# Optimization experiments

Measured on AMD Instinct MI355X. Metric: run time of the kernel, lower is better.

Reference implementation:

```python
import jax, jax.numpy as jnp
import numpy as np

DIM = 512
HEADS = 8
DIM_HEAD = 64
HIDDEN = HEADS * DIM_HEAD
SCALE = DIM_HEAD ** -0.5


def rmsnorm_ch(x, g):
    # F.normalize over channel dim (axis=1), then * g * sqrt(C)
    # x: [b, c, l], g: [c]
    n = jnp.maximum(jnp.linalg.norm(x, axis=1, keepdims=True), 1e-12)
    c = x.shape[1]
    return (x / n) * g[None, :, None] * (c ** 0.5)


def setup_inputs() -> dict:
    key = jax.random.key(0)
    ks = jax.random.split(key, 6)
    b, l = 8, 4096
    x = jax.random.normal(ks[0], (b, DIM, l), dtype=jnp.float32)
    g_in = jnp.ones((DIM,), dtype=jnp.float32)
    # conv1d kernel_size=1 == matmul; kaiming-ish init scale
    w_qkv = jax.random.normal(ks[1], (3 * HIDDEN, DIM), dtype=jnp.float32) * (1.0 / np.sqrt(DIM))
    w_out = jax.random.normal(ks[2], (DIM, HIDDEN), dtype=jnp.float32) * (1.0 / np.sqrt(HIDDEN))
    b_out = jax.random.normal(ks[3], (DIM,), dtype=jnp.float32) * 0.01
    g_out = jnp.ones((DIM,), dtype=jnp.float32)
    return {"x": x, "g_in": g_in, "w_qkv": w_qkv, "w_out": w_out, "b_out": b_out, "g_out": g_out}


def reference(x, g_in, w_qkv, w_out, b_out, g_out):
    b, c, l = x.shape
    residual = x
    xn = rmsnorm_ch(x, g_in)                       # [b, c, l]
    qkv = jnp.einsum('oc,bcl->bol', w_qkv, xn)     # [b, 3*hidden, l]
    q, k, v = jnp.split(qkv, 3, axis=1)            # each [b, hidden, l]
    def to_heads(t):
        return t.reshape(b, HEADS, DIM_HEAD, l)    # [b, h, d, l]
    q, k, v = to_heads(q), to_heads(k), to_heads(v)
    q = jax.nn.softmax(q, axis=2) * SCALE          # softmax over head-dim d
    k = jax.nn.softmax(k, axis=3)                  # softmax over sequence l
    context = jnp.einsum('bhdn,bhen->bhde', k, v)  # [b, h, d, e]
    out = jnp.einsum('bhde,bhdn->bhen', context, q)  # [b, h, e, l]
    out = out.reshape(b, HIDDEN, l)
    o = jnp.einsum('ch,bhl->bcl', w_out, out) + b_out[None, :, None]
    o = rmsnorm_ch(o, g_out)
    return o + residual
```

## Files before the change

### kernel.cpp

```cpp
#include <hip/hip_runtime.h>


#define BB 8
#define CC 512
#define LL 4096
#define HH 8
#define DH 64
#define TC 1536

__device__ __constant__ const float SQRT_C = 22.62741699796952f;
#define SCALE_Q 0.125f

typedef unsigned short bfr_t;
typedef __attribute__((ext_vector_type(8))) short short8;
typedef __attribute__((ext_vector_type(4))) float f32x4;

__device__ __forceinline__ float bf2f(bfr_t v) {
  union { unsigned u; float f; } c; c.u = ((unsigned)v) << 16; return c.f;
}
__device__ __forceinline__ bfr_t f2bf(float f) {
  union { float f; unsigned u; } c; c.f = f;
  unsigned u = c.u + 0x7fffu + ((c.u >> 16) & 1u);
  return (bfr_t)(u >> 16);
}

__device__ __forceinline__ void load_lds16(const bfr_t* g, short* l) {
  __builtin_amdgcn_global_load_lds(
      (const __attribute__((address_space(1))) void*)g,
      (__attribute__((address_space(3))) void*)l, 16, 0, 0);
}

__global__ __launch_bounds__(256) void conv_bf16_2(
    const float* __restrict__ in1, bfr_t* __restrict__ o1, int n1,
    const float* __restrict__ in2, bfr_t* __restrict__ o2, int n2) {
  int i8 = (blockIdx.x * 256 + threadIdx.x) * 8;
  const float* src;
  bfr_t* dst;
  if (i8 < n1) { src = in1 + i8; dst = o1 + i8; }
  else {
    int j8 = i8 - n1;
    if (j8 >= n2) return;
    src = in2 + j8; dst = o2 + j8;
  }
  f32x4 a = *(const f32x4*)src;
  f32x4 b = *(const f32x4*)(src + 4);
  union { short s[8]; f32x4 v; } pk;
#pragma unroll
  for (int u = 0; u < 4; ++u) { pk.s[u] = (short)f2bf(a[u]); pk.s[u + 4] = (short)f2bf(b[u]); }
  *(f32x4*)dst = pk.v;
}

__global__ __launch_bounds__(256) void fused_norm_transpose(
    const float* __restrict__ x, const float* __restrict__ g,
    bfr_t* __restrict__ xt) {
  __shared__ float tile[64][65];
  __shared__ float red[4][64];
  __shared__ float invn_s[64];
  int b = blockIdx.y, l0 = blockIdx.x * 64;
  int t = threadIdx.x, ll = t & 63, cg = t >> 6;
  const float* xb = x + (size_t)b * CC * LL + l0;
  float vals[8][16];
  float ss = 0.f;
#pragma unroll
  for (int ch = 0; ch < 8; ++ch) {
    int c0 = ch * 64;
#pragma unroll
    for (int i = 0; i < 16; ++i) {
      int c = i * 4 + cg;
      float v = xb[(size_t)(c0 + c) * LL + ll];
      vals[ch][i] = v;
      ss += v * v;
    }
  }
  red[cg][ll] = ss;
  __syncthreads();
  if (cg == 0) {
    float s = red[0][ll] + red[1][ll] + red[2][ll] + red[3][ll];
    invn_s[ll] = SQRT_C / fmaxf(sqrtf(s), 1e-12f);
  }
  __syncthreads();
  int lw = t >> 2, ccw = (t & 3) * 16;
  float iv = invn_s[lw];
#pragma unroll
  for (int ch = 0; ch < 8; ++ch) {
    int c0 = ch * 64;
#pragma unroll
    for (int i = 0; i < 16; ++i) tile[i * 4 + cg][ll] = vals[ch][i];
    __syncthreads();
    union { short s[16]; f32x4 v[2]; } pk;
#pragma unroll
    for (int u = 0; u < 16; ++u) {
      int c = ccw + u;
      pk.s[u] = (short)f2bf(tile[c][lw] * g[c0 + c] * iv);
    }
    bfr_t* dst = xt + ((size_t)b * LL + l0 + lw) * CC + c0 + ccw;
    *(f32x4*)dst = pk.v[0];
    *(f32x4*)(dst + 8) = pk.v[1];
    __syncthreads();
  }
}

#define NT 8

__device__ __forceinline__ void stage_half(const bfr_t* g, short* l, int wid) {
  load_lds16(g + (size_t)wid * 8192,        l + wid * 1024);
  load_lds16(g + (size_t)wid * 8192 + 4096, l + wid * 1024 + 512);
}

#define CFENCE asm volatile("" ::: "memory")
#define LGKM0 asm volatile("s_waitcnt lgkmcnt(0)" ::: "memory")
#define VMC0  asm volatile("s_waitcnt vmcnt(0)" ::: "memory")
#define SB    __builtin_amdgcn_sched_barrier(0)
#define BAR   do { CFENCE; __builtin_amdgcn_s_barrier(); CFENCE; } while (0)
#define PRIO1 __builtin_amdgcn_s_setprio(1)
#define PRIO0 __builtin_amdgcn_s_setprio(0)

#define DSR(dst, addr, LIT) \
  asm volatile("ds_read_b128 %0, %1 offset:" #LIT : "=v"(dst) : "v"(addr))

#define RD_A(S, L0, L1, L2, L3) do {           \
    DSR(S[0], aAs0, L0); DSR(S[1], aAs1, L0);  \
    DSR(S[2], aAs0, L1); DSR(S[3], aAs1, L1);  \
    DSR(S[4], aAs0, L2); DSR(S[5], aAs1, L2);  \
    DSR(S[6], aAs0, L3); DSR(S[7], aAs1, L3); } while (0)
#define RD_B(S, L0, L1) do {                   \
    DSR(S[0], bBs0, L0); DSR(S[1], bBs1, L0);  \
    DSR(S[2], bBs0, L1); DSR(S[3], bBs1, L1); } while (0)

#define MMA8(QM, QN, AS, BS) do {                                            \
    _Pragma("unroll") for (int i_ = 0; i_ < 4; ++i_)                         \
      _Pragma("unroll") for (int j_ = 0; j_ < 2; ++j_) {                     \
        acc[(QM)*4+i_][(QN)*2+j_] = __builtin_amdgcn_mfma_f32_16x16x32_bf16( \
            AS[i_*2+0], BS[j_*2+0], acc[(QM)*4+i_][(QN)*2+j_], 0, 0, 0);     \
        acc[(QM)*4+i_][(QN)*2+j_] = __builtin_amdgcn_mfma_f32_16x16x32_bf16( \
            AS[i_*2+1], BS[j_*2+1], acc[(QM)*4+i_][(QN)*2+j_], 0, 0, 0);     \
      }                                                                      \
  } while (0)

#define STAGE_T(J, D) do {                                                   \
    stage_half(pA0 + (J) * 64, As + (D) * 16384, wid);                       \
    stage_half(pA1 + (J) * 64, As + (D) * 16384 + 8192, wid);                \
    stage_half(pB0 + (J) * 64, Bs + (D) * 16384, wid);                       \
    stage_half(pB1 + (J) * 64, Bs + (D) * 16384 + 8192, wid);                \
  } while (0)

#define TILE_E(KT) do {                                                      \
    PRIO1; RD_B(bS1, 4096, 6144); MMA8(0, 0, aS0, bS0); PRIO0; LGKM0; SB;    \
    PRIO1; RD_A(aS1, 8192, 10240, 12288, 14336); MMA8(0, 1, aS0, bS1);      \
    PRIO0; LGKM0; SB;                                                        \
    if ((KT) < 7) { VMC0; }                                                  \
    BAR;                                                                     \
    if ((KT) <= 5) STAGE_T((KT) + 2, 0);                                     \
    PRIO1;                                                                   \
    if ((KT) < 7) RD_A(aS0, 32768, 34816, 36864, 38912);                     \
    MMA8(1, 1, aS1, bS1); PRIO0; LGKM0; SB;                                  \
    PRIO1; MMA8(1, 0, aS1, bS0); PRIO0;                                      \
    if ((KT) < 7) RD_B(bS0, 32768, 34816);                                   \
    LGKM0; SB;                                                               \
  } while (0)

#define TILE_O(KT) do {                                                      \
    PRIO1; RD_B(bS1, 36864, 38912); MMA8(0, 0, aS0, bS0); PRIO0; LGKM0; SB;  \
    PRIO1; RD_A(aS1, 40960, 43008, 45056, 47104); MMA8(0, 1, aS0, bS1);     \
    PRIO0; LGKM0; SB;                                                        \
    if ((KT) < 7) { VMC0; }                                                  \
    BAR;                                                                     \
    if ((KT) <= 5) STAGE_T((KT) + 2, 1);                                     \
    PRIO1;                                                                   \
    if ((KT) < 7) RD_A(aS0, 0, 2048, 4096, 6144);                            \
    MMA8(1, 1, aS1, bS1); PRIO0; LGKM0; SB;                                  \
    PRIO1; MMA8(1, 0, aS1, bS0); PRIO0;                                      \
    if ((KT) < 7) RD_B(bS0, 0, 2048);                                        \
    LGKM0; SB;                                                               \
  } while (0)

__global__ __launch_bounds__(512, 2) void gemm256(
    const bfr_t* __restrict__ A, const bfr_t* __restrict__ Bt,
    bfr_t* __restrict__ Cout, const float* __restrict__ bias, int M, int Mtot) {
  __shared__ short lds[65536];
  short* As = lds;
  short* Bs = lds + 32768;

  int nwg = gridDim.x;
  int gy = M >> 8;
  int bid = blockIdx.x;
  int logical = (bid & 7) * (nwg >> 3) + (bid >> 3);
  int perz = (LL / 256) * gy;
  int bz = logical / perz;
  int rem = logical - bz * perz;
  int bx = rem / gy;
  int by = rem - bx * gy;

  int m0 = by * 256, n0 = bx * 256;
  int t = threadIdx.x, lane = t & 63, wid = t >> 6;
  int quad = lane >> 4, r16 = lane & 15;
  int wm = wid >> 2, wn = wid & 3;
  int soff = (lane >> 3) * 512 + (((lane & 7) ^ (lane >> 3)) * 8);
  int slot0 = (quad ^ (lane & 7)) * 8;
  int slot1 = ((4 + quad) ^ (lane & 7)) * 8;

  unsigned lb = (unsigned)(uintptr_t)(__attribute__((address_space(3))) short*)lds;
  unsigned aAs0 = lb + (unsigned)(wm * 16384 + r16 * 128 + slot0 * 2);
  unsigned aAs1 = lb + (unsigned)(wm * 16384 + r16 * 128 + slot1 * 2);
  unsigned bbase = 65536u + (unsigned)((wn >> 1) * 16384 + ((wn & 1) * 64 + r16) * 128);
  unsigned bBs0 = lb + bbase + (unsigned)(slot0 * 2);
  unsigned bBs1 = lb + bbase + (unsigned)(slot1 * 2);

  const bfr_t* pA0 = A + (size_t)m0 * 512 + soff;
  const bfr_t* pA1 = pA0 + (size_t)128 * 512;
  const bfr_t* pB0 = Bt + (size_t)bz * LL * 512 + (size_t)n0 * 512 + soff;
  const bfr_t* pB1 = pB0 + (size_t)128 * 512;

  f32x4 acc[8][4] = {};
  short8 aS0[8], aS1[8];
  short8 bS0[4], bS1[4];

  STAGE_T(0, 0);
  STAGE_T(1, 1);
  asm volatile("s_waitcnt vmcnt(8)" ::: "memory");
  BAR;
  RD_A(aS0, 0, 2048, 4096, 6144);
  RD_B(bS0, 0, 2048);
  LGKM0; SB;

  TILE_E(0); TILE_O(1); TILE_E(2); TILE_O(3);
  TILE_E(4); TILE_O(5); TILE_E(6); TILE_O(7);

  bfr_t* Cb = Cout + (size_t)bz * Mtot * LL;
  int crow = m0 + wm * 128 + quad * 4;
  int ccol = n0 + wn * 64 + r16;
#pragma unroll
  for (int am = 0; am < 8; ++am) {
    int rbase = crow + (am >> 2) * 64 + (am & 3) * 16;
#pragma unroll
    for (int reg = 0; reg < 4; ++reg) {
      int row = rbase + reg;
      float bi = bias ? bias[row] : 0.f;
#pragma unroll
      for (int an = 0; an < 4; ++an) {
        int col = ccol + (an >> 1) * 32 + (an & 1) * 16;
        Cb[(size_t)row * LL + col] = f2bf(acc[am][an][reg] + bi);
      }
    }
  }
}

__global__ __launch_bounds__(256) void context_mfma(
    const bfr_t* __restrict__ qkv, float* __restrict__ ctx_p,
    float* __restrict__ ksum_p) {
  __shared__ float red[4][4096];
  int s = blockIdx.x, bh = blockIdx.y;
  int b = bh >> 3, h = bh & 7;
  int t = threadIdx.x, lane = t & 63, wid = t >> 6;
  int quad = lane >> 4, r = lane & 15;
  const bfr_t* kb = qkv + ((size_t)b * TC + 512 + h * 64) * LL;
  const bfr_t* vb = qkv + ((size_t)b * TC + 1024 + h * 64) * LL;
  int n_base = s * 512 + wid * 128;
  f32x4 acc[4][4] = {};
  float ps[4] = {};
#pragma unroll
  for (int ks = 0; ks < 4; ++ks) {
    int n0 = n_base + ks * 32;
    short8 af[4], bf8[4];
#pragma unroll
    for (int i = 0; i < 4; ++i) {
      union { short s[8]; short8 v8; } uk;
      uk.v8 = *(const short8*)&kb[(size_t)(i * 16 + r) * LL + n0 + quad * 8];
#pragma unroll
      for (int jj = 0; jj < 8; ++jj) {
        float e = __expf(bf2f((bfr_t)uk.s[jj]));
        uk.s[jj] = (short)f2bf(e);
        ps[i] += e;
      }
      af[i] = uk.v8;
      bf8[i] = *(const short8*)&vb[(size_t)(i * 16 + r) * LL + n0 + quad * 8];
    }
#pragma unroll
    for (int i = 0; i < 4; ++i)
#pragma unroll
      for (int j = 0; j < 4; ++j)
        acc[i][j] = __builtin_amdgcn_mfma_f32_16x16x32_bf16(af[i], bf8[j],
                                                            acc[i][j], 0, 0, 0);
  }
#pragma unroll
  for (int i = 0; i < 4; ++i) {
    ps[i] += __shfl_xor(ps[i], 16, 64);
    ps[i] += __shfl_xor(ps[i], 32, 64);
  }
  if (quad == 0) {
#pragma unroll
    for (int i = 0; i < 4; ++i) red[wid][i * 16 + r] = ps[i];
  }
  __syncthreads();
  if (t < 64)
    ksum_p[((size_t)bh * 8 + s) * 64 + t] =
        red[0][t] + red[1][t] + red[2][t] + red[3][t];
  __syncthreads();
#pragma unroll
  for (int i = 0; i < 4; ++i)
#pragma unroll
    for (int j = 0; j < 4; ++j)
#pragma unroll
      for (int reg = 0; reg < 4; ++reg)
        red[wid][(i * 16 + quad * 4 + reg) * 64 + j * 16 + r] = acc[i][j][reg];
  __syncthreads();
  float* out = ctx_p + ((size_t)bh * 8 + s) * 4096;
#pragma unroll
  for (int u = 0; u < 16; ++u) {
    int idx = u * 256 + t;
    out[idx] = red[0][idx] + red[1][idx] + red[2][idx] + red[3][idx];
  }
}

__global__ __launch_bounds__(256) void context_reduce(
    const float* __restrict__ ctx_p, const float* __restrict__ ksum_p,
    bfr_t* __restrict__ ctx_bf) {
  __shared__ float zinv[64];
  int bh = blockIdx.x;
  int t = threadIdx.x;
  if (t < 64) {
    float s = 0.f;
#pragma unroll
    for (int s8 = 0; s8 < 8; ++s8) s += ksum_p[((size_t)bh * 8 + s8) * 64 + t];
    zinv[t] = 1.f / s;
  }
  __syncthreads();
#pragma unroll
  for (int i = 0; i < 16; ++i) {
    int idx = i * 256 + t;
    int d = idx >> 6;
    float sum = 0.f;
#pragma unroll
    for (int s = 0; s < 8; ++s) sum += ctx_p[((size_t)bh * 8 + s) * 4096 + idx];
    ctx_bf[(size_t)bh * 4096 + idx] = f2bf(sum * zinv[d]);
  }
}

__global__ __launch_bounds__(256) void apply_fused(
    const bfr_t* __restrict__ qkv, const bfr_t* __restrict__ ctx_bf,
    bfr_t* __restrict__ out_t) {
  int b = blockIdx.z, h = blockIdx.y;
  int t = threadIdx.x, lane = t & 63, wid = t >> 6;
  int quad = lane >> 4, r = lane & 15;
  int n0 = blockIdx.x * 256 + wid * 64;
  const bfr_t* qb = qkv + ((size_t)b * TC + h * 64) * LL;
  const bfr_t* cb = ctx_bf + (size_t)(b * HH + h) * 4096;
  float v[4][16];
  float psum[4];
#pragma unroll
  for (int i = 0; i < 4; ++i) {
    float s = 0.f;
#pragma unroll
    for (int ks = 0; ks < 2; ++ks)
#pragma unroll
      for (int jj = 0; jj < 8; ++jj) {
        float q = bf2f(qb[(size_t)(ks * 32 + quad * 8 + jj) * LL + n0 + i * 16 + r]);
        float e = __expf(q);
        v[i][ks * 8 + jj] = e;
        s += e;
      }
    psum[i] = s;
  }
#pragma unroll
  for (int i = 0; i < 4; ++i) {
    psum[i] += __shfl_xor(psum[i], 16, 64);
    psum[i] += __shfl_xor(psum[i], 32, 64);
  }
  short8 af[2][4];
#pragma unroll
  for (int i = 0; i < 4; ++i) {
    float sc = SCALE_Q / psum[i];
#pragma unroll
    for (int ks = 0; ks < 2; ++ks) {
      union { short s[8]; short8 v8; } u;
#pragma unroll
      for (int jj = 0; jj < 8; ++jj) u.s[jj] = (short)f2bf(v[i][ks * 8 + jj] * sc);
      af[ks][i] = u.v8;
    }
  }
  short8 bfrag[2][4];
#pragma unroll
  for (int ks = 0; ks < 2; ++ks)
#pragma unroll
    for (int j = 0; j < 4; ++j) {
      union { short s[8]; short8 v8; } u;
#pragma unroll
      for (int jj = 0; jj < 8; ++jj)
        u.s[jj] = (short)cb[(ks * 32 + quad * 8 + jj) * 64 + j * 16 + r];
      bfrag[ks][j] = u.v8;
    }
  f32x4 acc[4][4] = {};
#pragma unroll
  for (int ks = 0; ks < 2; ++ks)
#pragma unroll
    for (int i = 0; i < 4; ++i)
#pragma unroll
      for (int j = 0; j < 4; ++j)
        acc[i][j] = __builtin_amdgcn_mfma_f32_16x16x32_bf16(af[ks][i], bfrag[ks][j],
                                                            acc[i][j], 0, 0, 0);
  bfr_t* dst = out_t + (size_t)b * LL * 512 + h * 64;
#pragma unroll
  for (int i = 0; i < 4; ++i)
#pragma unroll
    for (int reg = 0; reg < 4; ++reg) {
      int row = n0 + i * 16 + quad * 4 + reg;
#pragma unroll
      for (int j = 0; j < 4; ++j)
        dst[(size_t)row * 512 + j * 16 + r] = f2bf(acc[i][j][reg]);
    }
}

__global__ __launch_bounds__(256) void final_norm_res(
    const bfr_t* __restrict__ o, const float* __restrict__ g,
    const float* __restrict__ x, float* __restrict__ out) {
  __shared__ float red[4][128];
  __shared__ float invn[128];
  int b = blockIdx.y, l0 = blockIdx.x * 128;
  int t = threadIdx.x, ll = t & 63, cg = t >> 6;
  const bfr_t* ob = o + (size_t)b * CC * LL + l0 + ll * 2;
  float ss0 = 0.f, ss1 = 0.f;
  for (int c = cg * 128; c < cg * 128 + 128; ++c) {
    unsigned u = *(const unsigned*)&ob[(size_t)c * LL];
    float v0 = bf2f((bfr_t)(u & 0xffffu));
    float v1 = bf2f((bfr_t)(u >> 16));
    ss0 += v0 * v0;
    ss1 += v1 * v1;
  }
  red[cg][ll * 2] = ss0;
  red[cg][ll * 2 + 1] = ss1;
  __syncthreads();
  if (t < 128) {
    float s = red[0][t] + red[1][t] + red[2][t] + red[3][t];
    invn[t] = SQRT_C / fmaxf(sqrtf(s), 1e-12f);
  }
  __syncthreads();
  float iv0 = invn[ll * 2], iv1 = invn[ll * 2 + 1];
  const float* xb = x + (size_t)b * CC * LL + l0 + ll * 2;
  float* outb = out + (size_t)b * CC * LL + l0 + ll * 2;
  for (int c = cg * 128; c < cg * 128 + 128; ++c) {
    unsigned u = *(const unsigned*)&ob[(size_t)c * LL];
    float gc = g[c];
    float v0 = bf2f((bfr_t)(u & 0xffffu)) * gc * iv0;
    float v1 = bf2f((bfr_t)(u >> 16)) * gc * iv1;
    float2 xv = *(const float2*)&xb[(size_t)c * LL];
    float2 ov;
    ov.x = v0 + xv.x;
    ov.y = v1 + xv.y;
    *(float2*)&outb[(size_t)c * LL] = ov;
  }
}

extern "C" void kernel_launch(void* const* d_in, const int* in_sizes, int n_in,
                              void* d_out, int out_size, void* d_ws,
                              size_t ws_size, hipStream_t stream) {
  const float* x     = (const float*)d_in[0];
  const float* g_in  = (const float*)d_in[1];
  const float* w_qkv = (const float*)d_in[2];
  const float* w_out = (const float*)d_in[3];
  const float* b_out = (const float*)d_in[4];
  const float* g_out = (const float*)d_in[5];
  float* out = (float*)d_out;

  char* ws = (char*)d_ws;
  const size_t off_wqkv  = 0;
  const size_t off_wout  = 1572864;
  const size_t off_ksump = 2097152;
  const size_t off_ctx   = 2260992;
  const size_t off_ctxp  = 3309568;
  const size_t off_xt    = 11698176;
  const size_t off_qkv   = 45252608;
  const size_t ws_need   = 145915904;
  if (ws_size < ws_need) return;

  bfr_t* wqkv_bf = (bfr_t*)(ws + off_wqkv);
  bfr_t* wout_bf = (bfr_t*)(ws + off_wout);
  float* ksum_p  = (float*)(ws + off_ksump);
  bfr_t* ctx_bf  = (bfr_t*)(ws + off_ctx);
  float* ctxp    = (float*)(ws + off_ctxp);
  bfr_t* xt      = (bfr_t*)(ws + off_xt);
  bfr_t* qkv     = (bfr_t*)(ws + off_qkv);
  bfr_t* o_bf    = (bfr_t*)(ws + off_qkv);

  conv_bf16_2<<<dim3((1536 * 512 + 512 * 512) / 8 / 256), 256, 0, stream>>>(
      w_qkv, wqkv_bf, 1536 * 512, w_out, wout_bf, 512 * 512);
  fused_norm_transpose<<<dim3(LL / 64, BB), 256, 0, stream>>>(x, g_in, xt);
  for (int p = 0; p < 3; ++p)
    gemm256<<<dim3((LL / 256) * 2 * BB), 512, 0, stream>>>(
        wqkv_bf + (size_t)p * 512 * 512, xt, qkv + (size_t)p * 512 * LL,
        nullptr, 512, TC);
  context_mfma<<<dim3(8, BB * HH), 256, 0, stream>>>(qkv, ctxp, ksum_p);
  context_reduce<<<dim3(BB * HH), 256, 0, stream>>>(ctxp, ksum_p, ctx_bf);
  apply_fused<<<dim3(LL / 256, HH, BB), 256, 0, stream>>>(qkv, ctx_bf, xt);
  gemm256<<<dim3((LL / 256) * 2 * BB), 512, 0, stream>>>(wout_bf, xt, o_bf, b_out, 512, 512);
  final_norm_res<<<dim3(LL / 128, BB), 256, 0, stream>>>(o_bf, g_out, x, out);
}
```

Before: 299.2 us.

## Fuse output projection GEMM with channel RMSNorm and residual; merge QKV GEMM launches

Adds a new GEMM kernel for the output projection in which each workgroup owns all 512 output channels for a 128-column tile. It computes the bias, the per-column sum of squares, the RMS normalization and the residual add in its epilogue, so the bf16 intermediate no longer goes through HBM and the separate final_norm_res kernel is removed. The three per-slice QKV GEMM launches become a single launch over M=1536, and the Mtot parameter is dropped. The fused kernel uses a narrower N tile with full-M A staging and a larger LDS footprint (147KB). It also writes fp32 output with uncoalesced per-row scalar stores, which may limit the gain.

```diff
diff --git a/kernel.cpp b/kernel.cpp
--- a/kernel.cpp
+++ b/kernel.cpp
@@ -176,7 +176,7 @@
 
 __global__ __launch_bounds__(512, 2) void gemm256(
     const bfr_t* __restrict__ A, const bfr_t* __restrict__ Bt,
-    bfr_t* __restrict__ Cout, const float* __restrict__ bias, int M, int Mtot) {
+    bfr_t* __restrict__ Cout, const float* __restrict__ bias, int M) {
   __shared__ short lds[65536];
   short* As = lds;
   short* Bs = lds + 32768;
@@ -226,7 +226,7 @@
   TILE_E(0); TILE_O(1); TILE_E(2); TILE_O(3);
   TILE_E(4); TILE_O(5); TILE_E(6); TILE_O(7);
 
-  bfr_t* Cb = Cout + (size_t)bz * Mtot * LL;
+  bfr_t* Cb = Cout + (size_t)bz * M * LL;
   int crow = m0 + wm * 128 + quad * 4;
   int ccol = n0 + wn * 64 + r16;
 #pragma unroll
@@ -243,6 +243,141 @@
       }
     }
   }
+}
+
+#define WSTAGE_A(KT, DB) do {                                                \
+    _Pragma("unroll") for (int u_ = 0; u_ < 8; ++u_)                         \
+      load_lds16(gA + (size_t)(wid * 8 + u_) * 8 * 512 + (KT) * 64,          \
+                 lds + (DB) * 32768 + (wid * 8 + u_) * 512);                 \
+  } while (0)
+#define WSTAGE_B(KT) do {                                                    \
+    _Pragma("unroll") for (int u_ = 0; u_ < 2; ++u_)                         \
+      load_lds16(gB + (size_t)(wid * 2 + u_) * 8 * 512 + (KT) * 64,          \
+                 lds + 65536 + (wid * 2 + u_) * 512);                        \
+  } while (0)
+
+#define MMA_HF(H, AS) do {                                                   \
+    _Pragma("unroll") for (int i_ = 0; i_ < 4; ++i_)                         \
+      _Pragma("unroll") for (int j_ = 0; j_ < 4; ++j_) {                     \
+        acc[(H)*4+i_][j_] = __builtin_amdgcn_mfma_f32_16x16x32_bf16(         \
+            AS[i_*2+0], bS[j_*2+0], acc[(H)*4+i_][j_], 0, 0, 0);             \
+        acc[(H)*4+i_][j_] = __builtin_amdgcn_mfma_f32_16x16x32_bf16(         \
+            AS[i_*2+1], bS[j_*2+1], acc[(H)*4+i_][j_], 0, 0, 0);             \
+      }                                                                      \
+  } while (0)
+
+#define WTILE(KT, AB0, AB1) do {                                             \
+    DSR(bS[0], bR0, 0);    DSR(bS[1], bR1, 0);                               \
+    DSR(bS[2], bR0, 2048); DSR(bS[3], bR1, 2048);                            \
+    DSR(bS[4], bR0, 4096); DSR(bS[5], bR1, 4096);                            \
+    DSR(bS[6], bR0, 6144); DSR(bS[7], bR1, 6144);                            \
+    DSR(aS0[0], AB0, 0);    DSR(aS0[1], AB1, 0);                             \
+    DSR(aS0[2], AB0, 2048); DSR(aS0[3], AB1, 2048);                          \
+    DSR(aS0[4], AB0, 4096); DSR(aS0[5], AB1, 4096);                          \
+    DSR(aS0[6], AB0, 6144); DSR(aS0[7], AB1, 6144);                          \
+    LGKM0; SB; BAR;                                                          \
+    if ((KT) < 7) { WSTAGE_A((KT) + 1, ((KT) & 1) ^ 1); WSTAGE_B((KT) + 1); }\
+    PRIO1; MMA_HF(0, aS0); PRIO0;                                            \
+    DSR(aS1[0], AB0, 8192);  DSR(aS1[1], AB1, 8192);                         \
+    DSR(aS1[2], AB0, 10240); DSR(aS1[3], AB1, 10240);                        \
+    DSR(aS1[4], AB0, 12288); DSR(aS1[5], AB1, 12288);                        \
+    DSR(aS1[6], AB0, 14336); DSR(aS1[7], AB1, 14336);                        \
+    LGKM0; SB;                                                               \
+    PRIO1; MMA_HF(1, aS1); PRIO0;                                            \
+    if ((KT) < 7) { VMC0; BAR; }                                             \
+  } while (0)
+
+__global__ __launch_bounds__(512, 2) void gemm_wout_norm(
+    const bfr_t* __restrict__ A, const bfr_t* __restrict__ Bt,
+    const float* __restrict__ bias, const float* __restrict__ g,
+    const float* __restrict__ x, float* __restrict__ out) {
+  __shared__ short lds[73728];
+  int bid = blockIdx.x;
+  int bz = bid >> 5;
+  int l0 = (bid & 31) * 128;
+  int t = threadIdx.x, lane = t & 63, wid = t >> 6;
+  int quad = lane >> 4, r16 = lane & 15;
+  int wm = wid >> 1, wn = wid & 1;
+  int soff = (lane >> 3) * 512 + (((lane & 7) ^ (lane >> 3)) * 8);
+  int slot0 = (quad ^ (lane & 7)) * 16;
+  int slot1 = ((4 + quad) ^ (lane & 7)) * 16;
+
+  unsigned lb = (unsigned)(uintptr_t)(__attribute__((address_space(3))) short*)lds;
+  unsigned aR0b0 = lb + (unsigned)(wm * 16384 + r16 * 128 + slot0);
+  unsigned aR1b0 = lb + (unsigned)(wm * 16384 + r16 * 128 + slot1);
+  unsigned aR0b1 = aR0b0 + 65536u;
+  unsigned aR1b1 = aR1b0 + 65536u;
+  unsigned bR0 = lb + 131072u + (unsigned)(wn * 8192 + r16 * 128 + slot0);
+  unsigned bR1 = lb + 131072u + (unsigned)(wn * 8192 + r16 * 128 + slot1);
+
+  const bfr_t* gA = A + soff;
+  const bfr_t* gB = Bt + (size_t)bz * LL * 512 + (size_t)l0 * 512 + soff;
+
+  f32x4 acc[8][4] = {};
+  short8 aS0[8], aS1[8], bS[8];
+
+  WSTAGE_A(0, 0);
+  WSTAGE_B(0);
+  VMC0;
+  BAR;
+
+  WTILE(0, aR0b0, aR1b0); WTILE(1, aR0b1, aR1b1);
+  WTILE(2, aR0b0, aR1b0); WTILE(3, aR0b1, aR1b1);
+  WTILE(4, aR0b0, aR1b0); WTILE(5, aR0b1, aR1b1);
+  WTILE(6, aR0b0, aR1b0); WTILE(7, aR0b1, aR1b1);
+
+  __syncthreads();
+  float* redf = (float*)lds;
+  float* invf = (float*)lds + 512;
+  float ssl[4] = {0.f, 0.f, 0.f, 0.f};
+#pragma unroll
+  for (int am = 0; am < 8; ++am)
+#pragma unroll
+    for (int reg = 0; reg < 4; ++reg) {
+      int row = wm * 128 + (am >> 2) * 64 + (am & 3) * 16 + quad * 4 + reg;
+      float bi = bias[row];
+#pragma unroll
+      for (int an = 0; an < 4; ++an) {
+        float o = acc[am][an][reg] + bi;
+        ssl[an] += o * o;
+      }
+    }
+#pragma unroll
+  for (int an = 0; an < 4; ++an) {
+    ssl[an] += __shfl_xor(ssl[an], 16, 64);
+    ssl[an] += __shfl_xor(ssl[an], 32, 64);
+  }
+  if (quad == 0) {
+#pragma unroll
+    for (int an = 0; an < 4; ++an)
+      redf[wm * 128 + wn * 64 + an * 16 + r16] = ssl[an];
+  }
+  __syncthreads();
+  if (t < 128) {
+    float s = redf[t] + redf[128 + t] + redf[256 + t] + redf[384 + t];
+    invf[t] = SQRT_C / fmaxf(sqrtf(s), 1e-12f);
+  }
+  __syncthreads();
+  float iv[4];
+#pragma unroll
+  for (int an = 0; an < 4; ++an) iv[an] = invf[wn * 64 + an * 16 + r16];
+  const float* xb = x + (size_t)bz * CC * LL + l0;
+  float* ob = out + (size_t)bz * CC * LL + l0;
+  int cb = wn * 64 + r16;
+#pragma unroll
+  for (int am = 0; am < 8; ++am)
+#pragma unroll
+    for (int reg = 0; reg < 4; ++reg) {
+      int row = wm * 128 + (am >> 2) * 64 + (am & 3) * 16 + quad * 4 + reg;
+      float bi = bias[row], gr = g[row];
+      const float* xr = xb + (size_t)row * LL;
+      float* orow = ob + (size_t)row * LL;
+#pragma unroll
+      for (int an = 0; an < 4; ++an) {
+        int col = cb + an * 16;
+        orow[col] = (acc[am][an][reg] + bi) * gr * iv[an] + xr[col];
+      }
+    }
 }
 
 __global__ __launch_bounds__(256) void context_mfma(
@@ -410,46 +545,6 @@
     }
 }
 
-__global__ __launch_bounds__(256) void final_norm_res(
-    const bfr_t* __restrict__ o, const float* __restrict__ g,
-    const float* __restrict__ x, float* __restrict__ out) {
-  __shared__ float red[4][128];
-  __shared__ float invn[128];
-  int b = blockIdx.y, l0 = blockIdx.x * 128;
-  int t = threadIdx.x, ll = t & 63, cg = t >> 6;
-  const bfr_t* ob = o + (size_t)b * CC * LL + l0 + ll * 2;
-  float ss0 = 0.f, ss1 = 0.f;
-  for (int c = cg * 128; c < cg * 128 + 128; ++c) {
-    unsigned u = *(const unsigned*)&ob[(size_t)c * LL];
-    float v0 = bf2f((bfr_t)(u & 0xffffu));
-    float v1 = bf2f((bfr_t)(u >> 16));
-    ss0 += v0 * v0;
-    ss1 += v1 * v1;
-  }
-  red[cg][ll * 2] = ss0;
-  red[cg][ll * 2 + 1] = ss1;
-  __syncthreads();
-  if (t < 128) {
-    float s = red[0][t] + red[1][t] + red[2][t] + red[3][t];
-    invn[t] = SQRT_C / fmaxf(sqrtf(s), 1e-12f);
-  }
-  __syncthreads();
-  float iv0 = invn[ll * 2], iv1 = invn[ll * 2 + 1];
-  const float* xb = x + (size_t)b * CC * LL + l0 + ll * 2;
-  float* outb = out + (size_t)b * CC * LL + l0 + ll * 2;
-  for (int c = cg * 128; c < cg * 128 + 128; ++c) {
-    unsigned u = *(const unsigned*)&ob[(size_t)c * LL];
-    float gc = g[c];
-    float v0 = bf2f((bfr_t)(u & 0xffffu)) * gc * iv0;
-    float v1 = bf2f((bfr_t)(u >> 16)) * gc * iv1;
-    float2 xv = *(const float2*)&xb[(size_t)c * LL];
-    float2 ov;
-    ov.x = v0 + xv.x;
-    ov.y = v1 + xv.y;
-    *(float2*)&outb[(size_t)c * LL] = ov;
-  }
-}
-
 extern "C" void kernel_launch(void* const* d_in, const int* in_sizes, int n_in,
                               void* d_out, int out_size, void* d_ws,
                               size_t ws_size, hipStream_t stream) {
@@ -479,18 +574,14 @@
   float* ctxp    = (float*)(ws + off_ctxp);
   bfr_t* xt      = (bfr_t*)(ws + off_xt);
   bfr_t* qkv     = (bfr_t*)(ws + off_qkv);
-  bfr_t* o_bf    = (bfr_t*)(ws + off_qkv);
 
   conv_bf16_2<<<dim3((1536 * 512 + 512 * 512) / 8 / 256), 256, 0, stream>>>(
       w_qkv, wqkv_bf, 1536 * 512, w_out, wout_bf, 512 * 512);
   fused_norm_transpose<<<dim3(LL / 64, BB), 256, 0, stream>>>(x, g_in, xt);
-  for (int p = 0; p < 3; ++p)
-    gemm256<<<dim3((LL / 256) * 2 * BB), 512, 0, stream>>>(
-        wqkv_bf + (size_t)p * 512 * 512, xt, qkv + (size_t)p * 512 * LL,
-        nullptr, 512, TC);
+  gemm256<<<dim3((LL / 256) * (TC / 256) * BB), 512, 0, stream>>>(wqkv_bf, xt, qkv, nullptr, TC);
   context_mfma<<<dim3(8, BB * HH), 256, 0, stream>>>(qkv, ctxp, ksum_p);
   context_reduce<<<dim3(BB * HH), 256, 0, stream>>>(ctxp, ksum_p, ctx_bf);
   apply_fused<<<dim3(LL / 256, HH, BB), 256, 0, stream>>>(qkv, ctx_bf, xt);
-  gemm256<<<dim3((LL / 256) * 2 * BB), 512, 0, stream>>>(wout_bf, xt, o_bf, b_out, 512, 512);
-  final_norm_res<<<dim3(LL / 128, BB), 256, 0, stream>>>(o_bf, g_out, x, out);
-}
+  gemm_wout_norm<<<dim3((LL / 128) * BB), 512, 0, stream>>>(
+      wout_bf, xt, b_out, g_out, x, out);
+}
```

New measurement: 278.7 us. 6.8% less time.
